# Kernel tuning notes

Measured on AMD Instinct MI355X. Metric: run time of the kernel, lower is better.

Reference implementation:

```python
import jax, jax.numpy as jnp
import numpy as np

B, S, H = 2, 1024, 2048
E, K, I = 32, 4, 512   # num_experts, top_k, moe_intermediate
IS = 512               # shared_expert_intermediate


def setup_inputs() -> dict:
    key = jax.random.key(0)
    ks = jax.random.split(key, 10)
    s = 0.02
    return {
        "hidden_states": jax.random.normal(ks[0], (B, S, H), jnp.float32),
        "Wr": jax.random.normal(ks[1], (E, H), jnp.float32) * s,      # router gate
        "Wg": jax.random.normal(ks[2], (E, I, H), jnp.float32) * s,   # expert gate_proj
        "Wu": jax.random.normal(ks[3], (E, I, H), jnp.float32) * s,   # expert up_proj
        "Wd": jax.random.normal(ks[4], (E, H, I), jnp.float32) * s,   # expert down_proj
        "Wsg": jax.random.normal(ks[5], (IS, H), jnp.float32) * s,    # shared gate_proj
        "Wsu": jax.random.normal(ks[6], (IS, H), jnp.float32) * s,    # shared up_proj
        "Wsd": jax.random.normal(ks[7], (H, IS), jnp.float32) * s,    # shared down_proj
        "Wsgate": jax.random.normal(ks[8], (1, H), jnp.float32) * s,  # shared_expert_gate
    }


def reference(hidden_states, Wr, Wg, Wu, Wd, Wsg, Wsu, Wsd, Wsgate):
    b, s, h = hidden_states.shape
    x = hidden_states.reshape(-1, h)                      # [T, H]
    T = x.shape[0]

    # router: softmax in fp32, top-k, renormalize (norm_topk_prob=True)
    router_logits = x @ Wr.T                               # [T, E]
    rw = jax.nn.softmax(router_logits.astype(jnp.float32), axis=-1)
    vals, idx = jax.lax.top_k(rw, K)                       # [T, K]
    vals = vals / jnp.sum(vals, axis=-1, keepdims=True)
    vals = vals.astype(x.dtype)

    # combine-weight matrix: zeros except selected experts
    C = jnp.zeros((T, E), x.dtype).at[jnp.arange(T)[:, None], idx].add(vals)

    # all experts evaluate all tokens (calibrate_all_experts path); combine zeros non-selected
    g = jnp.einsum('th,eih->tei', x, Wg)                   # [T, E, I]
    u = jnp.einsum('th,eih->tei', x, Wu)
    hact = jax.nn.silu(g) * u
    moe_out = jnp.einsum('tei,ehi,te->th', hact, Wd, C)    # weighted combine

    # shared expert with sigmoid gate
    shared = (jax.nn.silu(x @ Wsg.T) * (x @ Wsu.T)) @ Wsd.T
    gate = jax.nn.sigmoid(x @ Wsgate.T)                    # [T, 1]
    out = (moe_out + gate * shared).reshape(b, s, h)
    return out, router_logits
```

## Files before the change

kernel.cpp:

```cpp
#include <hip/hip_runtime.h>
#include <math.h>

#define T_N 2048
#define H_N 2048
#define E_N 32
#define I_N 512
#define NA_MOE (T_N*4)
#define NA_ALL (NA_MOE + T_N)
#define BM 128
#define BK 32
#define MAXT 112

typedef short s16x8 __attribute__((ext_vector_type(8)));
typedef float f32x4 __attribute__((ext_vector_type(4)));

__device__ inline short f2bf(float f){
    unsigned int u = __float_as_uint(f);
    u = (u + 0x7fffu + ((u >> 16) & 1u)) >> 16;
    return (short)u;
}
__device__ inline float bf2f(short s){
    return __uint_as_float(((unsigned int)(unsigned short)s) << 16);
}
__device__ inline s16x8 cvt8(float4 f0, float4 f1){
    s16x8 v;
    v[0]=f2bf(f0.x); v[1]=f2bf(f0.y); v[2]=f2bf(f0.z); v[3]=f2bf(f0.w);
    v[4]=f2bf(f1.x); v[5]=f2bf(f1.y); v[6]=f2bf(f1.z); v[7]=f2bf(f1.w);
    return v;
}

__global__ __launch_bounds__(256) void cast_x_kernel(const float* __restrict__ x,
                                                     short* __restrict__ xbf){
    size_t i = (size_t)(blockIdx.x * 256 + threadIdx.x) * 8;
    float4 a = *(const float4*)(x + i);
    float4 b = *(const float4*)(x + i + 4);
    *(s16x8*)(xbf + i) = cvt8(a, b);
}

__global__ __launch_bounds__(64) void router_kernel(
    const float* __restrict__ x, const float* __restrict__ Wr,
    const float* __restrict__ Wsgate,
    float* __restrict__ logits_out, int* __restrict__ tidx, float* __restrict__ tw,
    int* __restrict__ perm, float* __restrict__ wgt, int* __restrict__ counts)
{
    const int t = blockIdx.x, lane = threadIdx.x;
    const float* xr = x + (size_t)t * H_N;
    float xv[32];
    #pragma unroll
    for (int i = 0; i < 32; i++) xv[i] = xr[i*64 + lane];
    __shared__ float lg[34];
    for (int e = 0; e < 33; e++){
        const float* wr = (e < 32) ? (Wr + (size_t)e * H_N) : Wsgate;
        double s = 0.0;
        #pragma unroll
        for (int i = 0; i < 32; i++) s += (double)xv[i] * (double)wr[i*64 + lane];
        #pragma unroll
        for (int o = 32; o > 0; o >>= 1) s += __shfl_down(s, o);
        if (lane == 0) lg[e] = (float)s;
    }
    __syncthreads();
    if (lane < 32) logits_out[(size_t)t*32 + lane] = lg[lane];
    if (lane == 0){
        float m = lg[0];
        for (int e = 1; e < 32; e++) m = fmaxf(m, lg[e]);
        unsigned mask = 0; int sel[4]; float sv[4]; float s4 = 0.f;
        for (int k = 0; k < 4; k++){
            int best = -1; float bv = -1e30f;
            for (int e = 0; e < 32; e++)
                if (!((mask >> e) & 1u) && lg[e] > bv){ bv = lg[e]; best = e; }
            mask |= 1u << best; sel[k] = best;
            float p = expf(lg[best] - m); sv[k] = p; s4 += p;
        }
        for (int k = 0; k < 4; k++){
            tidx[t*4 + k] = sel[k];
            tw[t*4 + k]   = sv[k] / s4;
            atomicAdd(&counts[sel[k]], 1);
        }
        perm[NA_MOE + t] = t;
        wgt[NA_MOE + t]  = 1.f / (1.f + expf(-lg[32]));
    }
}

__global__ void scan_kernel(int* ctrl){
    if (threadIdx.x == 0){
        int* counts = ctrl; int* eoff = ctrl + 128; int* ecnt = ctrl + 192;
        int acc = 0;
        for (int e = 0; e < 32; e++){ eoff[e] = acc; ecnt[e] = counts[e]; acc += counts[e]; }
        eoff[32] = NA_MOE; ecnt[32] = T_N;
        int nt = 0;
        for (int e = 0; e < 33; e++){
            int c = ecnt[e];
            for (int m = 0; m * BM < c; m++) ctrl[260 + nt++] = (e << 16) | m;
        }
        ctrl[256] = nt;
    }
    if (threadIdx.x < 64) ctrl[64 + threadIdx.x] = 0;
}

__global__ __launch_bounds__(256) void scatter_kernel(
    const int* __restrict__ tidx, const float* __restrict__ tw,
    int* __restrict__ perm, float* __restrict__ wgt, int* __restrict__ apos,
    int* ctrl)
{
    int t = blockIdx.x * 256 + threadIdx.x;
    if (t >= T_N) return;
    const int* eoff = ctrl + 128; int* cursor = ctrl + 64;
    for (int k = 0; k < 4; k++){
        int e = tidx[t*4 + k];
        int pos = eoff[e] + atomicAdd(&cursor[e], 1);
        perm[pos] = t; wgt[pos] = tw[t*4 + k]; apos[t*4 + k] = pos;
    }
}

__global__ __launch_bounds__(256, 3) void gemm1_kernel(
    const short* __restrict__ xbf,
    const float* __restrict__ Wg, const float* __restrict__ Wu,
    const float* __restrict__ Wsg, const float* __restrict__ Wsu,
    const int* __restrict__ perm, const int* __restrict__ ctrl,
    short* __restrict__ hact)
{
    const int tile = blockIdx.x >> 3;
    if (tile >= ctrl[256]) return;
    const int wrk = ctrl[260 + tile];
    const int e   = wrk >> 16;
    const int m0  = (wrk & 0xffff) << 7;
    const int cnt = ctrl[192 + e];
    const int off = ctrl[128 + e];
    const int n0  = (blockIdx.x & 7) << 6;

    __shared__ s16x8 lsA[4*128];
    __shared__ s16x8 lsBg[4*64];
    __shared__ s16x8 lsBu[4*64];

    const int tid = threadIdx.x;
    const int r_a = tid & 127;
    const int kca = tid >> 7;
    const short* arow = nullptr;
    if (m0 + r_a < cnt) arow = xbf + (size_t)perm[off + m0 + r_a] * H_N;

    const int rb = tid >> 2, kcb = tid & 3;
    const float *browg, *browu;
    if (e < 32){
        browg = Wg + ((size_t)e * I_N + (n0 + rb)) * H_N + kcb*8;
        browu = Wu + ((size_t)e * I_N + (n0 + rb)) * H_N + kcb*8;
    } else {
        browg = Wsg + (size_t)(n0 + rb) * H_N + kcb*8;
        browu = Wsu + (size_t)(n0 + rb) * H_N + kcb*8;
    }

    const int wid = tid >> 6, lane = tid & 63;
    const int wm = wid >> 1, wn = wid & 1;
    const int kg = lane >> 4, l15 = lane & 15;

    f32x4 accg[4][2], accu[4][2];
    #pragma unroll
    for (int a = 0; a < 4; a++)
        #pragma unroll
        for (int b = 0; b < 2; b++)
            #pragma unroll
            for (int j = 0; j < 4; j++){ accg[a][b][j] = 0.f; accu[a][b][j] = 0.f; }

    s16x8 a0{}, a1{};
    if (arow){
        a0 = *(const s16x8*)(arow + kca*8);
        a1 = *(const s16x8*)(arow + (kca+2)*8);
    }
    float4 g0 = *(const float4*)(browg);
    float4 g1 = *(const float4*)(browg + 4);
    float4 u0 = *(const float4*)(browu);
    float4 u1 = *(const float4*)(browu + 4);

    for (int k0 = 0; k0 < H_N; k0 += BK){
        __syncthreads();
        lsA[kca*128 + r_a]     = a0;
        lsA[(kca+2)*128 + r_a] = a1;
        lsBg[kcb*64 + rb]      = cvt8(g0, g1);
        lsBu[kcb*64 + rb]      = cvt8(u0, u1);
        __syncthreads();
        if (k0 + BK < H_N){
            if (arow){
                a0 = *(const s16x8*)(arow + k0 + BK + kca*8);
                a1 = *(const s16x8*)(arow + k0 + BK + (kca+2)*8);
            }
            g0 = *(const float4*)(browg + k0 + BK);
            g1 = *(const float4*)(browg + k0 + BK + 4);
            u0 = *(const float4*)(browu + k0 + BK);
            u1 = *(const float4*)(browu + k0 + BK + 4);
        }
        #pragma unroll
        for (int mf = 0; mf < 4; mf++){
            s16x8 a = lsA[kg*128 + wm*64 + mf*16 + l15];
            #pragma unroll
            for (int nf = 0; nf < 2; nf++){
                s16x8 bg = lsBg[kg*64 + wn*32 + nf*16 + l15];
                s16x8 bu = lsBu[kg*64 + wn*32 + nf*16 + l15];
                accg[mf][nf] = __builtin_amdgcn_mfma_f32_16x16x32_bf16(a, bg, accg[mf][nf], 0, 0, 0);
                accu[mf][nf] = __builtin_amdgcn_mfma_f32_16x16x32_bf16(a, bu, accu[mf][nf], 0, 0, 0);
            }
        }
    }
    #pragma unroll
    for (int mf = 0; mf < 4; mf++){
        #pragma unroll
        for (int j = 0; j < 4; j++){
            int row = m0 + wm*64 + mf*16 + kg*4 + j;
            if (row < cnt){
                #pragma unroll
                for (int nf = 0; nf < 2; nf++){
                    int col = n0 + wn*32 + nf*16 + l15;
                    float g = accg[mf][nf][j], u = accu[mf][nf][j];
                    float h = g / (1.f + expf(-g)) * u;
                    hact[(size_t)(off + row) * I_N + col] = f2bf(h);
                }
            }
        }
    }
}

template<int USE_Y>
__global__ __launch_bounds__(256) void gemm2_kernel(
    const short* __restrict__ hact,
    const float* __restrict__ Wd, const float* __restrict__ Wsd,
    const int* __restrict__ perm, const float* __restrict__ wgt,
    const int* __restrict__ ctrl, float* __restrict__ out, short* __restrict__ y)
{
    const int tile = blockIdx.x >> 5;
    if (tile >= ctrl[256]) return;
    const int wrk = ctrl[260 + tile];
    const int e   = wrk >> 16;
    const int m0  = (wrk & 0xffff) << 7;
    const int cnt = ctrl[192 + e];
    const int off = ctrl[128 + e];
    const int n0  = (blockIdx.x & 31) << 6;

    __shared__ s16x8 lsA[4*128];
    __shared__ s16x8 lsB[4*64];

    const int tid = threadIdx.x;
    const int r_a = tid & 127;
    const int kca = tid >> 7;
    const short* arow = nullptr;
    if (m0 + r_a < cnt) arow = hact + (size_t)(off + m0 + r_a) * I_N;

    const int rb = tid >> 2, kcb = tid & 3;
    const float* brow = (e < 32) ? (Wd  + ((size_t)e * H_N + (n0 + rb)) * I_N + kcb*8)
                                 : (Wsd + (size_t)(n0 + rb) * I_N + kcb*8);

    const int wid = tid >> 6, lane = tid & 63;
    const int wm = wid >> 1, wn = wid & 1;
    const int kg = lane >> 4, l15 = lane & 15;

    f32x4 acc[4][2];
    #pragma unroll
    for (int a = 0; a < 4; a++)
        #pragma unroll
        for (int b = 0; b < 2; b++)
            #pragma unroll
            for (int j = 0; j < 4; j++) acc[a][b][j] = 0.f;

    s16x8 a0{}, a1{};
    if (arow){
        a0 = *(const s16x8*)(arow + kca*8);
        a1 = *(const s16x8*)(arow + (kca+2)*8);
    }
    float4 f0 = *(const float4*)(brow);
    float4 f1 = *(const float4*)(brow + 4);

    for (int k0 = 0; k0 < I_N; k0 += BK){
        __syncthreads();
        lsA[kca*128 + r_a]     = a0;
        lsA[(kca+2)*128 + r_a] = a1;
        lsB[kcb*64 + rb]       = cvt8(f0, f1);
        __syncthreads();
        if (k0 + BK < I_N){
            if (arow){
                a0 = *(const s16x8*)(arow + k0 + BK + kca*8);
                a1 = *(const s16x8*)(arow + k0 + BK + (kca+2)*8);
            }
            f0 = *(const float4*)(brow + k0 + BK);
            f1 = *(const float4*)(brow + k0 + BK + 4);
        }
        #pragma unroll
        for (int mf = 0; mf < 4; mf++){
            s16x8 a = lsA[kg*128 + wm*64 + mf*16 + l15];
            #pragma unroll
            for (int nf = 0; nf < 2; nf++){
                s16x8 b = lsB[kg*64 + wn*32 + nf*16 + l15];
                acc[mf][nf] = __builtin_amdgcn_mfma_f32_16x16x32_bf16(a, b, acc[mf][nf], 0, 0, 0);
            }
        }
    }
    #pragma unroll
    for (int mf = 0; mf < 4; mf++){
        #pragma unroll
        for (int j = 0; j < 4; j++){
            int row = m0 + wm*64 + mf*16 + kg*4 + j;
            if (row < cnt){
                int aidx = off + row;
                if (USE_Y){
                    #pragma unroll
                    for (int nf = 0; nf < 2; nf++){
                        int col = n0 + wn*32 + nf*16 + l15;
                        y[(size_t)aidx * H_N + col] = f2bf(acc[mf][nf][j]);
                    }
                } else {
                    int tok = perm[aidx];
                    float w = wgt[aidx];
                    #pragma unroll
                    for (int nf = 0; nf < 2; nf++){
                        int col = n0 + wn*32 + nf*16 + l15;
                        atomicAdd(&out[(size_t)tok * H_N + col], w * acc[mf][nf][j]);
                    }
                }
            }
        }
    }
}

__global__ __launch_bounds__(256) void combine_kernel(
    const short* __restrict__ y, const int* __restrict__ apos,
    const float* __restrict__ tw, const float* __restrict__ wgt,
    float* __restrict__ out)
{
    const int t = blockIdx.x;
    const int c0 = threadIdx.x * 8;
    float acc[8];
    {
        float ws = wgt[NA_MOE + t];
        s16x8 v = *(const s16x8*)(y + (size_t)(NA_MOE + t) * H_N + c0);
        #pragma unroll
        for (int j = 0; j < 8; j++) acc[j] = ws * bf2f(v[j]);
    }
    #pragma unroll
    for (int k = 0; k < 4; k++){
        int p   = apos[t*4 + k];
        float w = tw[t*4 + k];
        s16x8 v = *(const s16x8*)(y + (size_t)p * H_N + c0);
        #pragma unroll
        for (int j = 0; j < 8; j++) acc[j] += w * bf2f(v[j]);
    }
    float4 o0 = make_float4(acc[0], acc[1], acc[2], acc[3]);
    float4 o1 = make_float4(acc[4], acc[5], acc[6], acc[7]);
    *(float4*)(out + (size_t)t * H_N + c0)     = o0;
    *(float4*)(out + (size_t)t * H_N + c0 + 4) = o1;
}

extern "C" void kernel_launch(void* const* d_in, const int* in_sizes, int n_in,
                              void* d_out, int out_size, void* d_ws, size_t ws_size,
                              hipStream_t stream)
{
    const float* x      = (const float*)d_in[0];
    const float* Wr     = (const float*)d_in[1];
    const float* Wg     = (const float*)d_in[2];
    const float* Wu     = (const float*)d_in[3];
    const float* Wd     = (const float*)d_in[4];
    const float* Wsg    = (const float*)d_in[5];
    const float* Wsu    = (const float*)d_in[6];
    const float* Wsd    = (const float*)d_in[7];
    const float* Wsgate = (const float*)d_in[8];

    float* out    = (float*)d_out;
    float* logits = out + (size_t)T_N * H_N;

    char* ws = (char*)d_ws;
    short* xbf  = (short*)ws;
    short* hact = (short*)(ws + 8388608);
    int*   perm = (int*)(ws + 18874368);
    float* wgt  = (float*)(ws + 18915328);
    int*   tidx = (int*)(ws + 18956288);
    float* tw   = (float*)(ws + 18989056);
    int*   apos = (int*)(ws + 19021824);
    int*   ctrl = (int*)(ws + 19054592);
    short* y    = (short*)(ws + 19056640);
    const size_t Y_END = 19056640ull + 41943040ull;
    const bool use_y = (ws_size >= Y_END);

    hipMemsetAsync(ctrl, 0, 256 * sizeof(int), stream);
    if (!use_y)
        hipMemsetAsync(d_out, 0, (size_t)T_N * H_N * sizeof(float), stream);

    cast_x_kernel<<<2048, 256, 0, stream>>>(x, xbf);
    router_kernel<<<T_N, 64, 0, stream>>>(x, Wr, Wsgate, logits, tidx, tw, perm, wgt, ctrl);
    scan_kernel<<<1, 64, 0, stream>>>(ctrl);
    scatter_kernel<<<T_N/256, 256, 0, stream>>>(tidx, tw, perm, wgt, apos, ctrl);
    gemm1_kernel<<<MAXT*8, 256, 0, stream>>>(xbf, Wg, Wu, Wsg, Wsu, perm, ctrl, hact);
    if (use_y){
        gemm2_kernel<1><<<MAXT*32, 256, 0, stream>>>(hact, Wd, Wsd, perm, wgt, ctrl, out, y);
        combine_kernel<<<T_N, 256, 0, stream>>>(y, apos, tw, wgt, out);
    } else {
        gemm2_kernel<0><<<MAXT*32, 256, 0, stream>>>(hact, Wd, Wsd, perm, wgt, ctrl, out, y);
    }
}
```

Baseline: 363.8 us.

## Double-buffer LDS tiles in both grouped GEMM kernels with two-stage prefetch

Both expert GEMM kernels now keep two LDS buffers and a two-deep register prefetch. Each iteration stores the next tile into the alternate buffer while MFMAs read the current one, so only one barrier per K step remains instead of two. gemm2 also gets a launch-bounds occupancy hint of 3 blocks per CU. The cost is double the LDS footprint and more live registers for the extra prefetch stage, which could reduce occupancy or cause spills.

```diff
diff --git a/kernel.cpp b/kernel.cpp
--- a/kernel.cpp
+++ b/kernel.cpp
@@ -128,9 +128,9 @@
     const int off = ctrl[128 + e];
     const int n0  = (blockIdx.x & 7) << 6;
 
-    __shared__ s16x8 lsA[4*128];
-    __shared__ s16x8 lsBg[4*64];
-    __shared__ s16x8 lsBu[4*64];
+    __shared__ s16x8 lsA[2][4*128];
+    __shared__ s16x8 lsBg[2][4*64];
+    __shared__ s16x8 lsBu[2][4*64];
 
     const int tid = threadIdx.x;
     const int r_a = tid & 127;
@@ -160,44 +160,68 @@
             #pragma unroll
             for (int j = 0; j < 4; j++){ accg[a][b][j] = 0.f; accu[a][b][j] = 0.f; }
 
-    s16x8 a0{}, a1{};
+    {
+        s16x8 a0{}, a1{};
+        if (arow){
+            a0 = *(const s16x8*)(arow + kca*8);
+            a1 = *(const s16x8*)(arow + (kca+2)*8);
+        }
+        lsA[0][kca*128 + r_a]     = a0;
+        lsA[0][(kca+2)*128 + r_a] = a1;
+        float4 g0 = *(const float4*)(browg);
+        float4 g1 = *(const float4*)(browg + 4);
+        float4 u0 = *(const float4*)(browu);
+        float4 u1 = *(const float4*)(browu + 4);
+        lsBg[0][kcb*64 + rb] = cvt8(g0, g1);
+        lsBu[0][kcb*64 + rb] = cvt8(u0, u1);
+    }
+    s16x8 pa0{}, pa1{};
     if (arow){
-        a0 = *(const s16x8*)(arow + kca*8);
-        a1 = *(const s16x8*)(arow + (kca+2)*8);
-    }
-    float4 g0 = *(const float4*)(browg);
-    float4 g1 = *(const float4*)(browg + 4);
-    float4 u0 = *(const float4*)(browu);
-    float4 u1 = *(const float4*)(browu + 4);
-
+        pa0 = *(const s16x8*)(arow + BK + kca*8);
+        pa1 = *(const s16x8*)(arow + BK + (kca+2)*8);
+    }
+    float4 pg0 = *(const float4*)(browg + BK);
+    float4 pg1 = *(const float4*)(browg + BK + 4);
+    float4 pu0 = *(const float4*)(browu + BK);
+    float4 pu1 = *(const float4*)(browu + BK + 4);
+
+    int cur = 0;
     for (int k0 = 0; k0 < H_N; k0 += BK){
         __syncthreads();
-        lsA[kca*128 + r_a]     = a0;
-        lsA[(kca+2)*128 + r_a] = a1;
-        lsBg[kcb*64 + rb]      = cvt8(g0, g1);
-        lsBu[kcb*64 + rb]      = cvt8(u0, u1);
-        __syncthreads();
+        s16x8 na0{}, na1{};
+        float4 ng0{}, ng1{}, nu0{}, nu1{};
+        if (k0 + 2*BK < H_N){
+            const int kn = k0 + 2*BK;
+            if (arow){
+                na0 = *(const s16x8*)(arow + kn + kca*8);
+                na1 = *(const s16x8*)(arow + kn + (kca+2)*8);
+            }
+            ng0 = *(const float4*)(browg + kn);
+            ng1 = *(const float4*)(browg + kn + 4);
+            nu0 = *(const float4*)(browu + kn);
+            nu1 = *(const float4*)(browu + kn + 4);
+        }
         if (k0 + BK < H_N){
-            if (arow){
-                a0 = *(const s16x8*)(arow + k0 + BK + kca*8);
-                a1 = *(const s16x8*)(arow + k0 + BK + (kca+2)*8);
-            }
-            g0 = *(const float4*)(browg + k0 + BK);
-            g1 = *(const float4*)(browg + k0 + BK + 4);
-            u0 = *(const float4*)(browu + k0 + BK);
-            u1 = *(const float4*)(browu + k0 + BK + 4);
+            const int nb = cur ^ 1;
+            lsA[nb][kca*128 + r_a]     = pa0;
+            lsA[nb][(kca+2)*128 + r_a] = pa1;
+            lsBg[nb][kcb*64 + rb] = cvt8(pg0, pg1);
+            lsBu[nb][kcb*64 + rb] = cvt8(pu0, pu1);
         }
         #pragma unroll
         for (int mf = 0; mf < 4; mf++){
-            s16x8 a = lsA[kg*128 + wm*64 + mf*16 + l15];
+            s16x8 a = lsA[cur][kg*128 + wm*64 + mf*16 + l15];
             #pragma unroll
             for (int nf = 0; nf < 2; nf++){
-                s16x8 bg = lsBg[kg*64 + wn*32 + nf*16 + l15];
-                s16x8 bu = lsBu[kg*64 + wn*32 + nf*16 + l15];
+                s16x8 bg = lsBg[cur][kg*64 + wn*32 + nf*16 + l15];
+                s16x8 bu = lsBu[cur][kg*64 + wn*32 + nf*16 + l15];
                 accg[mf][nf] = __builtin_amdgcn_mfma_f32_16x16x32_bf16(a, bg, accg[mf][nf], 0, 0, 0);
                 accu[mf][nf] = __builtin_amdgcn_mfma_f32_16x16x32_bf16(a, bu, accu[mf][nf], 0, 0, 0);
             }
         }
+        pa0 = na0; pa1 = na1;
+        pg0 = ng0; pg1 = ng1; pu0 = nu0; pu1 = nu1;
+        cur ^= 1;
     }
     #pragma unroll
     for (int mf = 0; mf < 4; mf++){
@@ -218,7 +242,7 @@
 }
 
 template<int USE_Y>
-__global__ __launch_bounds__(256) void gemm2_kernel(
+__global__ __launch_bounds__(256, 3) void gemm2_kernel(
     const short* __restrict__ hact,
     const float* __restrict__ Wd, const float* __restrict__ Wsd,
     const int* __restrict__ perm, const float* __restrict__ wgt,
@@ -233,8 +257,8 @@
     const int off = ctrl[128 + e];
     const int n0  = (blockIdx.x & 31) << 6;
 
-    __shared__ s16x8 lsA[4*128];
-    __shared__ s16x8 lsB[4*64];
+    __shared__ s16x8 lsA[2][4*128];
+    __shared__ s16x8 lsB[2][4*64];
 
     const int tid = threadIdx.x;
     const int r_a = tid & 127;
@@ -258,37 +282,57 @@
             #pragma unroll
             for (int j = 0; j < 4; j++) acc[a][b][j] = 0.f;
 
-    s16x8 a0{}, a1{};
+    {
+        s16x8 a0{}, a1{};
+        if (arow){
+            a0 = *(const s16x8*)(arow + kca*8);
+            a1 = *(const s16x8*)(arow + (kca+2)*8);
+        }
+        lsA[0][kca*128 + r_a]     = a0;
+        lsA[0][(kca+2)*128 + r_a] = a1;
+        float4 f0 = *(const float4*)(brow);
+        float4 f1 = *(const float4*)(brow + 4);
+        lsB[0][kcb*64 + rb] = cvt8(f0, f1);
+    }
+    s16x8 pa0{}, pa1{};
     if (arow){
-        a0 = *(const s16x8*)(arow + kca*8);
-        a1 = *(const s16x8*)(arow + (kca+2)*8);
-    }
-    float4 f0 = *(const float4*)(brow);
-    float4 f1 = *(const float4*)(brow + 4);
-
+        pa0 = *(const s16x8*)(arow + BK + kca*8);
+        pa1 = *(const s16x8*)(arow + BK + (kca+2)*8);
+    }
+    float4 pf0 = *(const float4*)(brow + BK);
+    float4 pf1 = *(const float4*)(brow + BK + 4);
+
+    int cur = 0;
     for (int k0 = 0; k0 < I_N; k0 += BK){
         __syncthreads();
-        lsA[kca*128 + r_a]     = a0;
-        lsA[(kca+2)*128 + r_a] = a1;
-        lsB[kcb*64 + rb]       = cvt8(f0, f1);
-        __syncthreads();
+        s16x8 na0{}, na1{};
+        float4 nf0{}, nf1{};
+        if (k0 + 2*BK < I_N){
+            const int kn = k0 + 2*BK;
+            if (arow){
+                na0 = *(const s16x8*)(arow + kn + kca*8);
+                na1 = *(const s16x8*)(arow + kn + (kca+2)*8);
+            }
+            nf0 = *(const float4*)(brow + kn);
+            nf1 = *(const float4*)(brow + kn + 4);
+        }
         if (k0 + BK < I_N){
-            if (arow){
-                a0 = *(const s16x8*)(arow + k0 + BK + kca*8);
-                a1 = *(const s16x8*)(arow + k0 + BK + (kca+2)*8);
-            }
-            f0 = *(const float4*)(brow + k0 + BK);
-            f1 = *(const float4*)(brow + k0 + BK + 4);
+            const int nb = cur ^ 1;
+            lsA[nb][kca*128 + r_a]     = pa0;
+            lsA[nb][(kca+2)*128 + r_a] = pa1;
+            lsB[nb][kcb*64 + rb] = cvt8(pf0, pf1);
         }
         #pragma unroll
         for (int mf = 0; mf < 4; mf++){
-            s16x8 a = lsA[kg*128 + wm*64 + mf*16 + l15];
+            s16x8 a = lsA[cur][kg*128 + wm*64 + mf*16 + l15];
             #pragma unroll
             for (int nf = 0; nf < 2; nf++){
-                s16x8 b = lsB[kg*64 + wn*32 + nf*16 + l15];
+                s16x8 b = lsB[cur][kg*64 + wn*32 + nf*16 + l15];
                 acc[mf][nf] = __builtin_amdgcn_mfma_f32_16x16x32_bf16(a, b, acc[mf][nf], 0, 0, 0);
             }
         }
+        pa0 = na0; pa1 = na1; pf0 = nf0; pf1 = nf1;
+        cur ^= 1;
     }
     #pragma unroll
     for (int mf = 0; mf < 4; mf++){
```

Result: no change. 366.6 us (+0.8%).
